# Optimization experiments

Measured on AMD Instinct MI355X. Metric: run time of the kernel, lower is better.

Reference implementation:

```python
import jax, jax.numpy as jnp
import numpy as np

DEGREE = 8


def _askey_wilson_basis(x, a, b, c, d, q, degree):
    # Iterative 3-term recurrence (same math as the recursive torch version).
    # x: (batch, input_dim); a,b,c,d,q: scalars broadcast over x.
    basis = [jnp.ones_like(x)]
    if degree >= 1:
        p1 = (2 * (1 + a * b * q) * x - (a + b) * (1 + c * d * q)) / (1 + a * b * c * d * q ** 2)
        basis.append(p1)
    for n in range(2, degree + 1):
        An = (1 - a * b * q ** (n - 1)) * (1 - c * d * q ** (n - 1)) * (1 - a * b * c * d * q ** (2 * n - 2))
        An = An / ((1 - a * b * c * d * q ** (2 * n - 1)) * (1 - a * b * c * d * q ** (2 * n)))
        Cn = (1 - q ** n) * (1 - a * b * q ** (n - 1)) * (1 - c * d * q ** (n - 1)) * (1 - a * b * c * d * q ** (2 * n - 2))
        Cn = Cn / ((1 - a * b * c * d * q ** (2 * n - 2)) * (1 - a * b * c * d * q ** (2 * n - 1)))
        pn = ((2 * x - An) * basis[n - 1] - Cn * basis[n - 2]) / (1 - q ** n)
        basis.append(pn)
    return jnp.stack(basis, axis=-1)  # (batch, input_dim, degree+1)


def setup_inputs() -> dict:
    key = jax.random.key(0)
    k1, k2, k3, k4, k5, k6, k7 = jax.random.split(key, 7)
    input_dim, output_dim, degree = 1024, 1024, DEGREE
    batch = 8192
    x = jax.random.normal(k1, (batch, input_dim), dtype=jnp.float32)
    a = jax.random.normal(k2, (1,), dtype=jnp.float32)
    b = jax.random.normal(k3, (1,), dtype=jnp.float32)
    c = jax.random.normal(k4, (1,), dtype=jnp.float32)
    d = jax.random.normal(k5, (1,), dtype=jnp.float32)
    q = jax.random.normal(k6, (1,), dtype=jnp.float32)
    std = 1.0 / (input_dim * (degree + 1))
    coeffs = jax.random.normal(k7, (input_dim, output_dim, degree + 1), dtype=jnp.float32) * std
    return {"x": x, "a": a, "b": b, "c": c, "d": d, "q": q, "coeffs": coeffs}


def reference(x, a, b, c, d, q, coeffs) -> jnp.ndarray:
    a0, b0, c0, d0, q0 = a[0], b[0], c[0], d[0], q[0]
    basis = _askey_wilson_basis(x, a0, b0, c0, d0, q0, DEGREE)  # (b, i, d+1)
    y = jnp.einsum('bid,iod->bo', basis, coeffs)
    return y
```

## Files before the change

kernel.cpp:

```cpp
#include <hip/hip_runtime.h>
#include <cstdint>

typedef unsigned short u16;
typedef __bf16 bf16x8 __attribute__((ext_vector_type(8)));
typedef float f32x4 __attribute__((ext_vector_type(4)));

#define M_DIM 8192
#define N_DIM 1024
#define I_DIM 1024
#define NDEG 8
#define K_DIM (I_DIM * NDEG)
#define BM 128
#define BN 128
#define BK 64
#define NT (K_DIM / BK)
#define A_TILE (BM * BK)
#define B_TILE (BN * BK)

__device__ __forceinline__ u16 f2bf(float f) {
    union { float f; uint32_t u; } v; v.f = f;
    return (u16)((v.u + 0x7FFFu + ((v.u >> 16) & 1u)) >> 16);
}

__device__ __forceinline__ void gload_lds16(const u16* g, u16* l) {
    auto lp = reinterpret_cast<__attribute__((address_space(3))) uint32_t*>(
        reinterpret_cast<uintptr_t>(l));
    __builtin_amdgcn_global_load_lds(reinterpret_cast<const uint32_t*>(g), lp, 16, 0, 0);
}

__device__ __forceinline__ void do_transform_block(
    int blk, int t, const float* __restrict__ coeffs,
    u16* __restrict__ Bt, float* __restrict__ bias, float (*lds)[292])
{
    int bi = blk >> 5, bo = blk & 31;
    int i0 = bi * 32, o0 = bo * 32;

    {
        int r = t >> 3, s = t & 7;
        const float4* src = (const float4*)(coeffs + ((size_t)(i0 + r) * N_DIM + o0) * 9);
#pragma unroll
        for (int j = 0; j < 9; ++j) {
            float4 v = src[s * 9 + j];
            *(float4*)&lds[r][(s * 9 + j) * 4] = v;
        }
    }
    __syncthreads();

    {
        int c = t >> 3, s2 = t & 7;
        u16 ob[32];
#pragma unroll
        for (int rr = 0; rr < 4; ++rr)
#pragma unroll
            for (int dd = 0; dd < 8; ++dd)
                ob[rr * 8 + dd] = f2bf(lds[s2 * 4 + rr][c * 9 + 1 + dd]);
        uint4* dst = (uint4*)(Bt + (size_t)(o0 + c) * K_DIM + (size_t)i0 * 8 + s2 * 32);
        const uint4* sp = (const uint4*)ob;
#pragma unroll
        for (int u = 0; u < 4; ++u) dst[u] = sp[u];
    }

    if (t < 32) {
        float sum = 0.f;
#pragma unroll
        for (int rr = 0; rr < 32; ++rr) sum += lds[rr][t * 9];
        atomicAdd(&bias[o0 + t], sum);
    }
}

__device__ __forceinline__ void do_basis_thread(
    int gt, const float* __restrict__ x,
    const float* __restrict__ pa, const float* __restrict__ pb,
    const float* __restrict__ pc, const float* __restrict__ pd,
    const float* __restrict__ pq, u16* __restrict__ A, int row0)
{
    int rb = gt >> 7;
    int g  = gt & 127;
    int i0 = g << 3;
    int b  = row0 + rb;

    float a = *pa, bb = *pb, c = *pc, d = *pd, q = *pq;
    float ab = a * bb, cd = c * d, abcd = ab * cd;

    float qp[17];
    qp[0] = 1.f;
#pragma unroll
    for (int k = 1; k <= 16; ++k) qp[k] = qp[k - 1] * q;

    float den1 = 1.f + abcd * q * q;
    float c1x = 2.f * (1.f + ab * q) / den1;
    float c1c = -(a + bb) * (1.f + cd * q) / den1;

    float An[9], Cn[9], Sn[9];
#pragma unroll
    for (int n = 2; n <= 8; ++n) {
        float t1 = 1.f - ab * qp[n - 1];
        float t2 = 1.f - cd * qp[n - 1];
        float t3 = 1.f - abcd * qp[2 * n - 2];
        float t4 = 1.f - abcd * qp[2 * n - 1];
        float t5 = 1.f - abcd * qp[2 * n];
        An[n] = (t1 * t2 * t3) / (t4 * t5);
        Cn[n] = ((1.f - qp[n]) * t1 * t2 * t3) / (t3 * t4);
        Sn[n] = 1.f / (1.f - qp[n]);
    }

    const float4* x4 = (const float4*)(x + (size_t)b * I_DIM + i0);
    float4 v0 = x4[0], v1 = x4[1];
    float xv[8] = {v0.x, v0.y, v0.z, v0.w, v1.x, v1.y, v1.z, v1.w};

    u16 ob[64];
#pragma unroll
    for (int j = 0; j < 8; ++j) {
        float xj = xv[j];
        float p1 = c1x * xj + c1c;
        ob[j * 8 + 0] = f2bf(p1);
        float pm2 = 1.f, pm1 = p1;
#pragma unroll
        for (int n = 2; n <= 8; ++n) {
            float pn = ((2.f * xj - An[n]) * pm1 - Cn[n] * pm2) * Sn[n];
            ob[j * 8 + n - 1] = f2bf(pn);
            pm2 = pm1; pm1 = pn;
        }
    }

    uint4* dst = (uint4*)(A + (size_t)rb * K_DIM + (size_t)i0 * 8);
    const uint4* s = (const uint4*)ob;
#pragma unroll
    for (int u = 0; u < 8; ++u) dst[u] = s[u];
}

__global__ __launch_bounds__(256) void aw_prep(
    const float* __restrict__ coeffs, const float* __restrict__ x,
    const float* __restrict__ pa, const float* __restrict__ pb,
    const float* __restrict__ pc, const float* __restrict__ pd,
    const float* __restrict__ pq,
    u16* __restrict__ Bt, float* __restrict__ bias, u16* __restrict__ A)
{
    __shared__ float lds[32][292];
    int blk = blockIdx.x;
    int t = threadIdx.x;
    if (blk < 1024) {
        do_transform_block(blk, t, coeffs, Bt, bias, lds);
    } else {
        int gt = (blk - 1024) * 256 + t;
        do_basis_thread(gt, x, pa, pb, pc, pd, pq, A, 0);
    }
}

__global__ __launch_bounds__(256) void aw_transform(
    const float* __restrict__ coeffs, u16* __restrict__ Bt, float* __restrict__ bias)
{
    __shared__ float lds[32][292];
    do_transform_block(blockIdx.x, threadIdx.x, coeffs, Bt, bias, lds);
}

__global__ void aw_basis(const float* __restrict__ x,
                         const float* __restrict__ pa, const float* __restrict__ pb,
                         const float* __restrict__ pc, const float* __restrict__ pd,
                         const float* __restrict__ pq,
                         u16* __restrict__ A, int row0)
{
    do_basis_thread(blockIdx.x * 256 + threadIdx.x, x, pa, pb, pc, pd, pq, A, row0);
}

__global__ __launch_bounds__(256) void aw_gemm(
    const u16* __restrict__ A,
    const u16* __restrict__ B,
    const float* __restrict__ bias,
    float* __restrict__ C,
    int row0, int rowBlocks)
{
    __shared__ alignas(16) u16 As[2 * A_TILE];
    __shared__ alignas(16) u16 Bs[2 * B_TILE];

    int nwg = rowBlocks * 8;
    int bid = blockIdx.x;
    int per = nwg >> 3;
    int logical = (bid & 7) * per + (bid >> 3);
    int rowBlk = logical >> 3;
    int colBlk = logical & 7;

    const int tid  = threadIdx.x;
    const int lane = tid & 63;
    const int wid  = tid >> 6;
    const int wr = wid >> 1;
    const int wc = wid & 1;

    const u16* gA[4]; const u16* gB[4];
    int ldsA[4], ldsB[4];
#pragma unroll
    for (int j = 0; j < 4; ++j) {
        int idx = j * 256 + tid;
        int r = idx >> 3, sl = idx & 7;
        gA[j] = A + (size_t)rowBlk * BM * K_DIM + (size_t)r * K_DIM + ((sl ^ (r & 7)) << 3);
        ldsA[j] = idx << 3;
        gB[j] = B + (size_t)colBlk * BN * K_DIM + (size_t)r * K_DIM + ((sl ^ (r & 7)) << 3);
        ldsB[j] = idx << 3;
    }

    int offA[2][4], offB[2][4];
#pragma unroll
    for (int ks = 0; ks < 2; ++ks) {
#pragma unroll
        for (int mi = 0; mi < 4; ++mi) {
            int r = wr * 64 + mi * 16 + (lane & 15);
            int s = ks * 4 + (lane >> 4);
            offA[ks][mi] = r * 128 + ((s ^ (r & 7)) << 4);
        }
#pragma unroll
        for (int ni = 0; ni < 4; ++ni) {
            int r = wc * 64 + ni * 16 + (lane & 15);
            int s = ks * 4 + (lane >> 4);
            offB[ks][ni] = r * 128 + ((s ^ (r & 7)) << 4);
        }
    }

    f32x4 acc[4][4];
#pragma unroll
    for (int mi = 0; mi < 4; ++mi)
#pragma unroll
        for (int ni = 0; ni < 4; ++ni)
            acc[mi][ni] = (f32x4){0.f, 0.f, 0.f, 0.f};

    auto stage = [&](int kt, int buf) {
        const int k0 = kt * BK;
        u16* dA = As + buf * A_TILE;
        u16* dB = Bs + buf * B_TILE;
        gload_lds16(gA[0] + k0, dA + ldsA[0]);
        gload_lds16(gA[1] + k0, dA + ldsA[1]);
        gload_lds16(gA[2] + k0, dA + ldsA[2]);
        gload_lds16(gA[3] + k0, dA + ldsA[3]);
        gload_lds16(gB[0] + k0, dB + ldsB[0]);
        gload_lds16(gB[1] + k0, dB + ldsB[1]);
        gload_lds16(gB[2] + k0, dB + ldsB[2]);
        gload_lds16(gB[3] + k0, dB + ldsB[3]);
    };

    stage(0, 0);
    asm volatile("s_waitcnt vmcnt(0)" ::: "memory");
    __builtin_amdgcn_s_barrier();

    for (int t = 0; t < NT; ++t) {
        const bool pf = (t + 1 < NT);
        if (pf) stage(t + 1, (t + 1) & 1);

        const char* aB = (const char*)(As + (t & 1) * A_TILE);
        const char* bB = (const char*)(Bs + (t & 1) * B_TILE);

        bf16x8 a0[4], b0[4], a1[4], b1[4];
#pragma unroll
        for (int mi = 0; mi < 4; ++mi) a0[mi] = *(const bf16x8*)(aB + offA[0][mi]);
#pragma unroll
        for (int ni = 0; ni < 4; ++ni) b0[ni] = *(const bf16x8*)(bB + offB[0][ni]);
#pragma unroll
        for (int mi = 0; mi < 4; ++mi) a1[mi] = *(const bf16x8*)(aB + offA[1][mi]);
#pragma unroll
        for (int ni = 0; ni < 4; ++ni) b1[ni] = *(const bf16x8*)(bB + offB[1][ni]);

        __builtin_amdgcn_s_setprio(1);
#pragma unroll
        for (int mi = 0; mi < 4; ++mi)
#pragma unroll
            for (int ni = 0; ni < 4; ++ni)
                acc[mi][ni] = __builtin_amdgcn_mfma_f32_16x16x32_bf16(
                    a0[mi], b0[ni], acc[mi][ni], 0, 0, 0);
#pragma unroll
        for (int mi = 0; mi < 4; ++mi)
#pragma unroll
            for (int ni = 0; ni < 4; ++ni)
                acc[mi][ni] = __builtin_amdgcn_mfma_f32_16x16x32_bf16(
                    a1[mi], b1[ni], acc[mi][ni], 0, 0, 0);
        __builtin_amdgcn_s_setprio(0);

        if (pf) {
            asm volatile("s_waitcnt vmcnt(0)" ::: "memory");
            __builtin_amdgcn_s_barrier();
        }
    }

    int gRow = row0 + rowBlk * BM + wr * 64;
    int gCol = colBlk * BN + wc * 64;
#pragma unroll
    for (int mi = 0; mi < 4; ++mi) {
#pragma unroll
        for (int ni = 0; ni < 4; ++ni) {
            int rr = gRow + mi * 16 + ((lane >> 4) << 2);
            int cc = gCol + ni * 16 + (lane & 15);
            float bv = bias[cc];
            float* dst = C + (size_t)rr * N_DIM + cc;
#pragma unroll
            for (int j = 0; j < 4; ++j) dst[(size_t)j * N_DIM] = acc[mi][ni][j] + bv;
        }
    }
}

extern "C" void kernel_launch(void* const* d_in, const int* in_sizes, int n_in,
                              void* d_out, int out_size, void* d_ws, size_t ws_size,
                              hipStream_t stream)
{
    const float* x      = (const float*)d_in[0];
    const float* pa     = (const float*)d_in[1];
    const float* pb     = (const float*)d_in[2];
    const float* pc     = (const float*)d_in[3];
    const float* pd     = (const float*)d_in[4];
    const float* pq     = (const float*)d_in[5];
    const float* coeffs = (const float*)d_in[6];
    float* out = (float*)d_out;

    float* bias = (float*)d_ws;
    const size_t biasBytes = 4096;
    u16* Bt = (u16*)((char*)d_ws + biasBytes);
    const size_t btBytes = (size_t)N_DIM * K_DIM * sizeof(u16);
    u16* Abuf = (u16*)((char*)d_ws + biasBytes + btBytes);
    size_t used = biasBytes + btBytes;
    size_t avail = ws_size > used ? ws_size - used : 0;
    const size_t aFullBytes = (size_t)M_DIM * K_DIM * sizeof(u16);

    hipMemsetAsync(bias, 0, N_DIM * sizeof(float), stream);

    if (avail >= aFullBytes) {
        aw_prep<<<1024 + (M_DIM * 128) / 256, 256, 0, stream>>>(
            coeffs, x, pa, pb, pc, pd, pq, Bt, bias, Abuf);
        aw_gemm<<<(M_DIM / BM) * 8, 256, 0, stream>>>(Abuf, Bt, bias, out, 0, M_DIM / BM);
    } else {
        int chunk = M_DIM;
        while (chunk > 256 && (size_t)chunk * K_DIM * sizeof(u16) > avail) chunk >>= 1;
        aw_transform<<<1024, 256, 0, stream>>>(coeffs, Bt, bias);
        for (int row0 = 0; row0 < M_DIM; row0 += chunk) {
            aw_basis<<<(chunk * 128) / 256, 256, 0, stream>>>(x, pa, pb, pc, pd, pq, Abuf, row0);
            aw_gemm<<<(chunk / BM) * 8, 256, 0, stream>>>(Abuf, Bt, bias, out, row0, chunk / BM);
        }
    }
}
```

Baseline: 201.4 us.

## Use 256x256 GEMM tiles with split-K across two halves plus reduce kernel

Doubles the GEMM block tile to 256x256 (8x8 MFMA fragments per wave, one wave per SIMD) to raise arithmetic intensity and cut global/LDS traffic per FLOP. To keep enough workgroups with the larger tiles, it splits K in two when workspace allows, writing the second half to a partial buffer. A new reduce kernel then adds the partial and the bias. Risks include high register pressure from 256 accumulators per thread, extra fp32 output traffic for the partial and reduce pass, and LDS usage of 128KB for the double buffers.

```diff
diff --git a/kernel.cpp b/kernel.cpp
--- a/kernel.cpp
+++ b/kernel.cpp
@@ -10,10 +10,10 @@
 #define I_DIM 1024
 #define NDEG 8
 #define K_DIM (I_DIM * NDEG)
-#define BM 128
-#define BN 128
+#define BM 256
+#define BN 256
 #define BK 64
-#define NT (K_DIM / BK)
+#define NT_FULL (K_DIM / BK)
 #define A_TILE (BM * BK)
 #define B_TILE (BN * BK)
 
@@ -163,22 +163,30 @@
     do_basis_thread(blockIdx.x * 256 + threadIdx.x, x, pa, pb, pc, pd, pq, A, row0);
 }
 
-__global__ __launch_bounds__(256) void aw_gemm(
+__global__ __launch_bounds__(256, 1) void aw_gemm(
     const u16* __restrict__ A,
     const u16* __restrict__ B,
-    const float* __restrict__ bias,
     float* __restrict__ C,
-    int row0, int rowBlocks)
+    float* __restrict__ part1,
+    int row0, int rowBlocks, int khSplit)
 {
     __shared__ alignas(16) u16 As[2 * A_TILE];
     __shared__ alignas(16) u16 Bs[2 * B_TILE];
 
-    int nwg = rowBlocks * 8;
+    int nwg = rowBlocks * 4 * khSplit;
     int bid = blockIdx.x;
-    int per = nwg >> 3;
-    int logical = (bid & 7) * per + (bid >> 3);
-    int rowBlk = logical >> 3;
-    int colBlk = logical & 7;
+    int logical = bid;
+    if ((nwg & 7) == 0) {
+        int per = nwg >> 3;
+        logical = (bid & 7) * per + (bid >> 3);
+    }
+    int rowBlk = logical / (4 * khSplit);
+    int rem    = logical - rowBlk * (4 * khSplit);
+    int colBlk = rem / khSplit;
+    int kh     = rem - colBlk * khSplit;
+
+    const int nTiles = NT_FULL / khSplit;
+    const int kBase  = kh * nTiles * BK;
 
     const int tid  = threadIdx.x;
     const int lane = tid & 63;
@@ -186,91 +194,77 @@
     const int wr = wid >> 1;
     const int wc = wid & 1;
 
-    const u16* gA[4]; const u16* gB[4];
-    int ldsA[4], ldsB[4];
-#pragma unroll
-    for (int j = 0; j < 4; ++j) {
+    const u16* gA[8]; const u16* gB[8];
+#pragma unroll
+    for (int j = 0; j < 8; ++j) {
         int idx = j * 256 + tid;
         int r = idx >> 3, sl = idx & 7;
-        gA[j] = A + (size_t)rowBlk * BM * K_DIM + (size_t)r * K_DIM + ((sl ^ (r & 7)) << 3);
-        ldsA[j] = idx << 3;
-        gB[j] = B + (size_t)colBlk * BN * K_DIM + (size_t)r * K_DIM + ((sl ^ (r & 7)) << 3);
-        ldsB[j] = idx << 3;
-    }
-
-    int offA[2][4], offB[2][4];
-#pragma unroll
-    for (int ks = 0; ks < 2; ++ks) {
-#pragma unroll
-        for (int mi = 0; mi < 4; ++mi) {
-            int r = wr * 64 + mi * 16 + (lane & 15);
-            int s = ks * 4 + (lane >> 4);
-            offA[ks][mi] = r * 128 + ((s ^ (r & 7)) << 4);
-        }
-#pragma unroll
-        for (int ni = 0; ni < 4; ++ni) {
-            int r = wc * 64 + ni * 16 + (lane & 15);
-            int s = ks * 4 + (lane >> 4);
-            offB[ks][ni] = r * 128 + ((s ^ (r & 7)) << 4);
-        }
-    }
-
-    f32x4 acc[4][4];
-#pragma unroll
-    for (int mi = 0; mi < 4; ++mi)
-#pragma unroll
-        for (int ni = 0; ni < 4; ++ni)
+        int col = ((sl ^ (r & 7)) << 3);
+        gA[j] = A + (size_t)(rowBlk * BM + r) * K_DIM + kBase + col;
+        gB[j] = B + (size_t)(colBlk * BN + r) * K_DIM + kBase + col;
+    }
+    const int ldsOff = tid << 3;
+
+    int offA[8], offB[8];
+#pragma unroll
+    for (int mi = 0; mi < 8; ++mi) {
+        int r = wr * 128 + mi * 16 + (lane & 15);
+        int s = (lane >> 4);
+        offA[mi] = r * 128 + ((s ^ (r & 7)) << 4);
+    }
+#pragma unroll
+    for (int ni = 0; ni < 8; ++ni) {
+        int r = wc * 128 + ni * 16 + (lane & 15);
+        int s = (lane >> 4);
+        offB[ni] = r * 128 + ((s ^ (r & 7)) << 4);
+    }
+
+    f32x4 acc[8][8];
+#pragma unroll
+    for (int mi = 0; mi < 8; ++mi)
+#pragma unroll
+        for (int ni = 0; ni < 8; ++ni)
             acc[mi][ni] = (f32x4){0.f, 0.f, 0.f, 0.f};
 
     auto stage = [&](int kt, int buf) {
         const int k0 = kt * BK;
         u16* dA = As + buf * A_TILE;
         u16* dB = Bs + buf * B_TILE;
-        gload_lds16(gA[0] + k0, dA + ldsA[0]);
-        gload_lds16(gA[1] + k0, dA + ldsA[1]);
-        gload_lds16(gA[2] + k0, dA + ldsA[2]);
-        gload_lds16(gA[3] + k0, dA + ldsA[3]);
-        gload_lds16(gB[0] + k0, dB + ldsB[0]);
-        gload_lds16(gB[1] + k0, dB + ldsB[1]);
-        gload_lds16(gB[2] + k0, dB + ldsB[2]);
-        gload_lds16(gB[3] + k0, dB + ldsB[3]);
+#pragma unroll
+        for (int j = 0; j < 8; ++j) gload_lds16(gA[j] + k0, dA + ldsOff + j * 2048);
+#pragma unroll
+        for (int j = 0; j < 8; ++j) gload_lds16(gB[j] + k0, dB + ldsOff + j * 2048);
     };
 
     stage(0, 0);
     asm volatile("s_waitcnt vmcnt(0)" ::: "memory");
     __builtin_amdgcn_s_barrier();
 
-    for (int t = 0; t < NT; ++t) {
-        const bool pf = (t + 1 < NT);
+    for (int t = 0; t < nTiles; ++t) {
+        const bool pf = (t + 1 < nTiles);
         if (pf) stage(t + 1, (t + 1) & 1);
 
         const char* aB = (const char*)(As + (t & 1) * A_TILE);
         const char* bB = (const char*)(Bs + (t & 1) * B_TILE);
 
-        bf16x8 a0[4], b0[4], a1[4], b1[4];
-#pragma unroll
-        for (int mi = 0; mi < 4; ++mi) a0[mi] = *(const bf16x8*)(aB + offA[0][mi]);
-#pragma unroll
-        for (int ni = 0; ni < 4; ++ni) b0[ni] = *(const bf16x8*)(bB + offB[0][ni]);
-#pragma unroll
-        for (int mi = 0; mi < 4; ++mi) a1[mi] = *(const bf16x8*)(aB + offA[1][mi]);
-#pragma unroll
-        for (int ni = 0; ni < 4; ++ni) b1[ni] = *(const bf16x8*)(bB + offB[1][ni]);
-
-        __builtin_amdgcn_s_setprio(1);
-#pragma unroll
-        for (int mi = 0; mi < 4; ++mi)
-#pragma unroll
-            for (int ni = 0; ni < 4; ++ni)
-                acc[mi][ni] = __builtin_amdgcn_mfma_f32_16x16x32_bf16(
-                    a0[mi], b0[ni], acc[mi][ni], 0, 0, 0);
-#pragma unroll
-        for (int mi = 0; mi < 4; ++mi)
-#pragma unroll
-            for (int ni = 0; ni < 4; ++ni)
-                acc[mi][ni] = __builtin_amdgcn_mfma_f32_16x16x32_bf16(
-                    a1[mi], b1[ni], acc[mi][ni], 0, 0, 0);
-        __builtin_amdgcn_s_setprio(0);
+#pragma unroll
+        for (int ks = 0; ks < 2; ++ks) {
+            const int x1 = ks ? 64 : 0;
+            bf16x8 fa[8], fb[8];
+#pragma unroll
+            for (int mi = 0; mi < 8; ++mi) fa[mi] = *(const bf16x8*)(aB + (offA[mi] ^ x1));
+#pragma unroll
+            for (int ni = 0; ni < 8; ++ni) fb[ni] = *(const bf16x8*)(bB + (offB[ni] ^ x1));
+
+            __builtin_amdgcn_s_setprio(1);
+#pragma unroll
+            for (int mi = 0; mi < 8; ++mi)
+#pragma unroll
+                for (int ni = 0; ni < 8; ++ni)
+                    acc[mi][ni] = __builtin_amdgcn_mfma_f32_16x16x32_bf16(
+                        fa[mi], fb[ni], acc[mi][ni], 0, 0, 0);
+            __builtin_amdgcn_s_setprio(0);
+        }
 
         if (pf) {
             asm volatile("s_waitcnt vmcnt(0)" ::: "memory");
@@ -278,19 +272,35 @@
         }
     }
 
-    int gRow = row0 + rowBlk * BM + wr * 64;
-    int gCol = colBlk * BN + wc * 64;
-#pragma unroll
-    for (int mi = 0; mi < 4; ++mi) {
-#pragma unroll
-        for (int ni = 0; ni < 4; ++ni) {
+    float* dstBase = (kh == 0) ? C : part1;
+    int gRow = row0 + rowBlk * BM + wr * 128;
+    int gCol = colBlk * BN + wc * 128;
+#pragma unroll
+    for (int mi = 0; mi < 8; ++mi) {
+#pragma unroll
+        for (int ni = 0; ni < 8; ++ni) {
             int rr = gRow + mi * 16 + ((lane >> 4) << 2);
             int cc = gCol + ni * 16 + (lane & 15);
-            float bv = bias[cc];
-            float* dst = C + (size_t)rr * N_DIM + cc;
-#pragma unroll
-            for (int j = 0; j < 4; ++j) dst[(size_t)j * N_DIM] = acc[mi][ni][j] + bv;
-        }
+            float* dst = dstBase + (size_t)rr * N_DIM + cc;
+#pragma unroll
+            for (int j = 0; j < 4; ++j) dst[(size_t)j * N_DIM] = acc[mi][ni][j];
+        }
+    }
+}
+
+__global__ __launch_bounds__(256) void aw_reduce(
+    float* __restrict__ out, const float* __restrict__ part1,
+    const float* __restrict__ bias, int addPart)
+{
+    const int total4 = M_DIM * N_DIM / 4;
+    f32x4* o4 = (f32x4*)out;
+    const f32x4* p4 = (const f32x4*)part1;
+    const f32x4* b4 = (const f32x4*)bias;
+    for (int i = blockIdx.x * 256 + threadIdx.x; i < total4; i += gridDim.x * 256) {
+        f32x4 v = o4[i];
+        if (addPart) v += p4[i];
+        v += b4[i & (N_DIM / 4 - 1)];
+        o4[i] = v;
     }
 }
 
@@ -312,23 +322,32 @@
     u16* Bt = (u16*)((char*)d_ws + biasBytes);
     const size_t btBytes = (size_t)N_DIM * K_DIM * sizeof(u16);
     u16* Abuf = (u16*)((char*)d_ws + biasBytes + btBytes);
+    const size_t aFullBytes = (size_t)M_DIM * K_DIM * sizeof(u16);
+    const size_t partBytes  = (size_t)M_DIM * N_DIM * sizeof(float);
     size_t used = biasBytes + btBytes;
     size_t avail = ws_size > used ? ws_size - used : 0;
-    const size_t aFullBytes = (size_t)M_DIM * K_DIM * sizeof(u16);
 
     hipMemsetAsync(bias, 0, N_DIM * sizeof(float), stream);
 
     if (avail >= aFullBytes) {
+        float* part1 = (float*)((char*)d_ws + biasBytes + btBytes + aFullBytes);
+        int khSplit = (avail >= aFullBytes + partBytes) ? 2 : 1;
+
         aw_prep<<<1024 + (M_DIM * 128) / 256, 256, 0, stream>>>(
             coeffs, x, pa, pb, pc, pd, pq, Bt, bias, Abuf);
-        aw_gemm<<<(M_DIM / BM) * 8, 256, 0, stream>>>(Abuf, Bt, bias, out, 0, M_DIM / BM);
+        int rowBlocks = M_DIM / BM;
+        aw_gemm<<<rowBlocks * 4 * khSplit, 256, 0, stream>>>(
+            Abuf, Bt, out, part1, 0, rowBlocks, khSplit);
+        aw_reduce<<<2048, 256, 0, stream>>>(out, part1, bias, khSplit == 2 ? 1 : 0);
     } else {
         int chunk = M_DIM;
         while (chunk > 256 && (size_t)chunk * K_DIM * sizeof(u16) > avail) chunk >>= 1;
         aw_transform<<<1024, 256, 0, stream>>>(coeffs, Bt, bias);
         for (int row0 = 0; row0 < M_DIM; row0 += chunk) {
             aw_basis<<<(chunk * 128) / 256, 256, 0, stream>>>(x, pa, pb, pc, pd, pq, Abuf, row0);
-            aw_gemm<<<(chunk / BM) * 8, 256, 0, stream>>>(Abuf, Bt, bias, out, row0, chunk / BM);
-        }
-    }
-}
+            aw_gemm<<<(chunk / BM) * 4, 256, 0, stream>>>(
+                Abuf, Bt, out, out, row0, chunk / BM, 1);
+        }
+        aw_reduce<<<2048, 256, 0, stream>>>(out, out, bias, 0);
+    }
+}
```

Measured after the change: 202.3 us. About the same (+0.4%).
